# Performance work log

Measured on AMD Instinct MI355X. Metric: run time of the kernel, lower is better.

## Reference

```python
import jax, jax.numpy as jnp
import numpy as np

N_NODES = 50000


def sage_conv(x, src, dst, Wl, bl, Wr):
    # PyG SAGEConv (aggr='mean'): out = lin_l(mean_{j in N(i)} x_j) + lin_r(x_i)
    # lin_l has bias, lin_r (root) has no bias.
    n = x.shape[0]
    agg = jax.ops.segment_sum(x[src], dst, num_segments=n)          # [N, d_in]
    cnt = jax.ops.segment_sum(jnp.ones((src.shape[0],), x.dtype), dst, num_segments=n)
    mean = agg / jnp.maximum(cnt, 1.0)[:, None]
    return mean @ Wl + bl + x @ Wr


def setup_inputs() -> dict:
    key = jax.random.key(0)
    k1, k2, k3, k4, k5, k6, k7 = jax.random.split(key, 7)
    in_c, hid_c, out_c = 128, 128, 2
    x = jax.random.normal(k1, (N_NODES, in_c), dtype=jnp.float32)
    edge_index = jax.random.randint(k2, (2, 800000), 0, N_NODES, dtype=jnp.int64)
    s1 = 1.0 / np.sqrt(in_c)
    s2 = 1.0 / np.sqrt(hid_c)
    return {
        "x": x,
        "edge_index": edge_index,
        "W1l": jax.random.uniform(k3, (in_c, hid_c), jnp.float32, -s1, s1),
        "b1l": jnp.zeros((hid_c,), jnp.float32),
        "W1r": jax.random.uniform(k4, (in_c, hid_c), jnp.float32, -s1, s1),
        "W2l": jax.random.uniform(k5, (hid_c, out_c), jnp.float32, -s2, s2),
        "b2l": jnp.zeros((out_c,), jnp.float32),
        "W2r": jax.random.uniform(k6, (hid_c, out_c), jnp.float32, -s2, s2),
    }


def reference(x, edge_index, W1l, b1l, W1r, W2l, b2l, W2r):
    src, dst = edge_index[0], edge_index[1]
    h = jax.nn.relu(sage_conv(x, src, dst, W1l, b1l, W1r))
    return sage_conv(h, src, dst, W2l, b2l, W2r)
```

## Files before the change

### kernel.cpp

```cpp
#include <hip/hip_runtime.h>

#define N_NODES 50000
#define N_PAD 50176
#define N_EDGES 800000
#define C 128
#define CAP 48
#define BUCK_B 391
#define PACK_B 16
#define TOBF_B 6250

typedef unsigned short ushort_t;
typedef unsigned int uint_t;
typedef __attribute__((ext_vector_type(8))) short bf16x8;
typedef __attribute__((ext_vector_type(4))) float f32x4;

__device__ __forceinline__ uint_t f2bf(float f) {
    uint_t u = __float_as_uint(f);
    u += 0x7fffu + ((u >> 16) & 1u);
    return u >> 16;
}
__device__ __forceinline__ float bflo(uint_t u) { return __uint_as_float(u << 16); }
__device__ __forceinline__ float bfhi(uint_t u) { return __uint_as_float(u & 0xffff0000u); }

__global__ __launch_bounds__(256) void bucketpack_kernel(
    const int* __restrict__ src, const int* __restrict__ dst,
    int* __restrict__ cursor, int* __restrict__ epad,
    const float* __restrict__ W1l, const float* __restrict__ W1r,
    ushort_t* __restrict__ Bp) {
    int b = blockIdx.x;
    if (b < BUCK_B) {
        int i4 = b * 256 + threadIdx.x;
        if (i4 < N_EDGES / 8) {
            int4 s0 = ((const int4*)src)[2 * i4];
            int4 s1 = ((const int4*)src)[2 * i4 + 1];
            int4 d0 = ((const int4*)dst)[2 * i4];
            int4 d1 = ((const int4*)dst)[2 * i4 + 1];
            int p0 = atomicAdd(&cursor[d0.x], 1);
            int p1 = atomicAdd(&cursor[d0.y], 1);
            int p2 = atomicAdd(&cursor[d0.z], 1);
            int p3 = atomicAdd(&cursor[d0.w], 1);
            int p4 = atomicAdd(&cursor[d1.x], 1);
            int p5 = atomicAdd(&cursor[d1.y], 1);
            int p6 = atomicAdd(&cursor[d1.z], 1);
            int p7 = atomicAdd(&cursor[d1.w], 1);
            if (p0 < CAP) epad[d0.x * CAP + p0] = s0.x;
            if (p1 < CAP) epad[d0.y * CAP + p1] = s0.y;
            if (p2 < CAP) epad[d0.z * CAP + p2] = s0.z;
            if (p3 < CAP) epad[d0.w * CAP + p3] = s0.w;
            if (p4 < CAP) epad[d1.x * CAP + p4] = s1.x;
            if (p5 < CAP) epad[d1.y * CAP + p5] = s1.y;
            if (p6 < CAP) epad[d1.z * CAP + p6] = s1.z;
            if (p7 < CAP) epad[d1.w * CAP + p7] = s1.w;
        }
    } else {
        int p = (b - BUCK_B) * 256 + threadIdx.x;
        int lane = p & 63;
        int pair = p >> 6;
        int kk = pair & 7;
        int nt = pair >> 3;
        int n = lane & 15, quad = lane >> 4;
        int col = nt * 16 + n;
        int k0 = kk * 32 + quad * 8;
        uint_t w[4];
        #pragma unroll
        for (int jj = 0; jj < 4; jj++) {
            int ka = k0 + 2 * jj, kb = k0 + 2 * jj + 1;
            float fa = (ka < C) ? W1l[ka * C + col] : W1r[(ka - C) * C + col];
            float fb = (kb < C) ? W1l[kb * C + col] : W1r[(kb - C) * C + col];
            w[jj] = f2bf(fa) | (f2bf(fb) << 16);
        }
        ((uint4*)(Bp + (size_t)p * 8))[0] = make_uint4(w[0], w[1], w[2], w[3]);
    }
}

__global__ __launch_bounds__(256) void tobf16_kernel(const float* __restrict__ x,
                                                     ushort_t* __restrict__ xh) {
    int i = blockIdx.x * 256 + threadIdx.x;
    float4 v = ((const float4*)x)[i];
    uint_t lo = f2bf(v.x) | (f2bf(v.y) << 16);
    uint_t hi = f2bf(v.z) | (f2bf(v.w) << 16);
    ((uint2*)xh)[i] = make_uint2(lo, hi);
}

__device__ __forceinline__ void bf8_acc(float* a, const uint4 v) {
    a[0] += bflo(v.x); a[1] += bfhi(v.x);
    a[2] += bflo(v.y); a[3] += bfhi(v.y);
    a[4] += bflo(v.z); a[5] += bfhi(v.z);
    a[6] += bflo(v.w); a[7] += bfhi(v.w);
}

__global__ __launch_bounds__(256) void gather_kernel(const ushort_t* __restrict__ xh,
                                                     const int* __restrict__ cursor,
                                                     const int* __restrict__ epad,
                                                     ushort_t* __restrict__ msb) {
    int t = threadIdx.x;
    int slot = t >> 4, q = t & 15;
    int node = blockIdx.x * 16 + slot;
    int d = cursor[node];
    int dd = d < CAP ? d : CAP;
    const int* lst = epad + node * CAP;
    float a[8] = {0,0,0,0,0,0,0,0};
    float b[8] = {0,0,0,0,0,0,0,0};
    int e = 0;
    for (; e + 8 <= dd; e += 8) {
        int s0 = lst[e + 0], s1 = lst[e + 1], s2 = lst[e + 2], s3 = lst[e + 3];
        int s4 = lst[e + 4], s5 = lst[e + 5], s6 = lst[e + 6], s7 = lst[e + 7];
        uint4 v0 = ((const uint4*)(xh + (size_t)s0 * C))[q];
        uint4 v1 = ((const uint4*)(xh + (size_t)s1 * C))[q];
        uint4 v2 = ((const uint4*)(xh + (size_t)s2 * C))[q];
        uint4 v3 = ((const uint4*)(xh + (size_t)s3 * C))[q];
        uint4 v4 = ((const uint4*)(xh + (size_t)s4 * C))[q];
        uint4 v5 = ((const uint4*)(xh + (size_t)s5 * C))[q];
        uint4 v6 = ((const uint4*)(xh + (size_t)s6 * C))[q];
        uint4 v7 = ((const uint4*)(xh + (size_t)s7 * C))[q];
        bf8_acc(a, v0); bf8_acc(b, v1); bf8_acc(a, v2); bf8_acc(b, v3);
        bf8_acc(a, v4); bf8_acc(b, v5); bf8_acc(a, v6); bf8_acc(b, v7);
    }
    for (; e + 4 <= dd; e += 4) {
        int s0 = lst[e + 0], s1 = lst[e + 1], s2 = lst[e + 2], s3 = lst[e + 3];
        uint4 v0 = ((const uint4*)(xh + (size_t)s0 * C))[q];
        uint4 v1 = ((const uint4*)(xh + (size_t)s1 * C))[q];
        uint4 v2 = ((const uint4*)(xh + (size_t)s2 * C))[q];
        uint4 v3 = ((const uint4*)(xh + (size_t)s3 * C))[q];
        bf8_acc(a, v0); bf8_acc(b, v1); bf8_acc(a, v2); bf8_acc(b, v3);
    }
    for (; e < dd; e++) {
        uint4 v = ((const uint4*)(xh + (size_t)lst[e] * C))[q];
        bf8_acc(a, v);
    }
    float inv = 1.0f / fmaxf((float)d, 1.0f);
    uint4 o;
    o.x = f2bf((a[0] + b[0]) * inv) | (f2bf((a[1] + b[1]) * inv) << 16);
    o.y = f2bf((a[2] + b[2]) * inv) | (f2bf((a[3] + b[3]) * inv) << 16);
    o.z = f2bf((a[4] + b[4]) * inv) | (f2bf((a[5] + b[5]) * inv) << 16);
    o.w = f2bf((a[6] + b[6]) * inv) | (f2bf((a[7] + b[7]) * inv) << 16);
    ((uint4*)(msb + (size_t)node * C))[q] = o;
}

__global__ __launch_bounds__(512) void gemm_mfma(
    const ushort_t* __restrict__ msb, const ushort_t* __restrict__ xh,
    const ushort_t* __restrict__ Bp, const float* __restrict__ b1l,
    const float* __restrict__ W2l, const float* __restrict__ W2r,
    const float* __restrict__ b2l, float* __restrict__ z, float* __restrict__ out) {
    __shared__ ushort_t sB[2 * C * C];
    int t = threadIdx.x;
    #pragma unroll
    for (int i = 0; i < 8; i++)
        ((uint4*)sB)[i * 512 + t] = ((const uint4*)Bp)[i * 512 + t];
    __syncthreads();

    int wid = t >> 6, lane = t & 63;
    int m = lane & 15, quad = lane >> 4;
    int base = blockIdx.x * 128 + wid * 16;

    const ushort_t* a_ms = msb + (size_t)(base + m) * C + quad * 8;
    const ushort_t* a_xh = xh  + (size_t)(base + m) * C + quad * 8;
    bf16x8 aw[8];
    #pragma unroll
    for (int kk = 0; kk < 4; kk++) aw[kk]     = *(const bf16x8*)(a_ms + kk * 32);
    #pragma unroll
    for (int kk = 0; kk < 4; kk++) aw[4 + kk] = *(const bf16x8*)(a_xh + kk * 32);

    f32x4 acc[8];
    #pragma unroll
    for (int nt = 0; nt < 8; nt++) acc[nt] = (f32x4){0.f, 0.f, 0.f, 0.f};

    const bf16x8* bp = (const bf16x8*)sB;
    #pragma unroll
    for (int kk = 0; kk < 8; kk++) {
        bf16x8 a = aw[kk];
        #pragma unroll
        for (int nt = 0; nt < 8; nt++) {
            bf16x8 bfr = bp[(nt * 8 + kk) * 64 + lane];
            acc[nt] = __builtin_amdgcn_mfma_f32_16x16x32_bf16(a, bfr, acc[nt], 0, 0, 0);
        }
    }

    float zz0[4] = {0,0,0,0}, zz1[4] = {0,0,0,0};
    float rr0[4] = {0,0,0,0}, rr1[4] = {0,0,0,0};
    #pragma unroll
    for (int nt = 0; nt < 8; nt++) {
        int col = nt * 16 + m;
        float bias = b1l[col];
        float2 wl = ((const float2*)W2l)[col];
        float2 wr = ((const float2*)W2r)[col];
        #pragma unroll
        for (int reg = 0; reg < 4; reg++) {
            float h = fmaxf(acc[nt][reg] + bias, 0.0f);
            zz0[reg] = fmaf(h, wl.x, zz0[reg]);
            zz1[reg] = fmaf(h, wl.y, zz1[reg]);
            rr0[reg] = fmaf(h, wr.x, rr0[reg]);
            rr1[reg] = fmaf(h, wr.y, rr1[reg]);
        }
    }
    float bl0 = b2l[0], bl1 = b2l[1];
    #pragma unroll
    for (int reg = 0; reg < 4; reg++) {
        float a0 = zz0[reg], a1 = zz1[reg], c0 = rr0[reg], c1 = rr1[reg];
        #pragma unroll
        for (int off = 8; off > 0; off >>= 1) {
            a0 += __shfl_down(a0, off, 16);
            a1 += __shfl_down(a1, off, 16);
            c0 += __shfl_down(c0, off, 16);
            c1 += __shfl_down(c1, off, 16);
        }
        if (m == 0) {
            int node = base + quad * 4 + reg;
            if (node < N_NODES) {
                z[node * 2 + 0]   = a0;
                z[node * 2 + 1]   = a1;
                out[node * 2 + 0] = c0 + bl0;
                out[node * 2 + 1] = c1 + bl1;
            }
        }
    }
}

__global__ __launch_bounds__(256) void final_kernel(const float* __restrict__ z,
                                                    const int* __restrict__ cursor,
                                                    const int* __restrict__ epad,
                                                    float* __restrict__ out) {
    int t = threadIdx.x;
    int sub = t & 15;
    int node = blockIdx.x * 16 + (t >> 4);
    int d = cursor[node];
    int dd = d < CAP ? d : CAP;
    const int* lst = epad + node * CAP;
    float a0 = 0.0f, a1 = 0.0f;
    for (int e = sub; e < dd; e += 16) {
        float2 v = ((const float2*)z)[lst[e]];
        a0 += v.x; a1 += v.y;
    }
    #pragma unroll
    for (int off = 8; off > 0; off >>= 1) {
        a0 += __shfl_down(a0, off);
        a1 += __shfl_down(a1, off);
    }
    if (sub == 0) {
        float inv = 1.0f / fmaxf((float)d, 1.0f);
        out[node * 2 + 0] += a0 * inv;
        out[node * 2 + 1] += a1 * inv;
    }
}

extern "C" void kernel_launch(void* const* d_in, const int* in_sizes, int n_in,
                              void* d_out, int out_size, void* d_ws, size_t ws_size,
                              hipStream_t stream) {
    const float* x   = (const float*)d_in[0];
    const int*   ei  = (const int*)d_in[1];
    const float* W1l = (const float*)d_in[2];
    const float* b1l = (const float*)d_in[3];
    const float* W1r = (const float*)d_in[4];
    const float* W2l = (const float*)d_in[5];
    const float* b2l = (const float*)d_in[6];
    const float* W2r = (const float*)d_in[7];
    float* out = (float*)d_out;

    const int* src = ei;
    const int* dst = ei + N_EDGES;

    int* cursor   = (int*)d_ws;
    int* epad     = cursor + N_PAD;
    ushort_t* xh  = (ushort_t*)(epad + N_NODES * CAP);
    ushort_t* msb = xh + (size_t)N_PAD * C;
    ushort_t* Bp  = msb + (size_t)N_PAD * C;
    float* z      = (float*)(Bp + 2 * C * C);

    hipMemsetAsync(cursor, 0, N_NODES * sizeof(int), stream);

    bucketpack_kernel<<<BUCK_B + PACK_B, 256, 0, stream>>>(
        src, dst, cursor, epad, W1l, W1r, Bp);
    tobf16_kernel<<<TOBF_B, 256, 0, stream>>>(x, xh);
    gather_kernel<<<N_NODES / 16, 256, 0, stream>>>(xh, cursor, epad, msb);
    gemm_mfma<<<392, 512, 0, stream>>>(
        msb, xh, Bp, b1l, W2l, W2r, b2l, z, out);
    final_kernel<<<N_NODES / 16, 256, 0, stream>>>(z, cursor, epad, out);
}
```

Baseline: 176.1 us.

## Replace per-node global atomic bucketing with two-pass coarse/fine bucket sort

New measurement: 157.8 us. -10.4%, faster.

```diff
diff --git a/kernel.cpp b/kernel.cpp
--- a/kernel.cpp
+++ b/kernel.cpp
@@ -5,9 +5,11 @@
 #define N_EDGES 800000
 #define C 128
 #define CAP 48
-#define BUCK_B 391
+#define NB 196
+#define CBCAP 4608
+#define B1_BUCK 391
+#define TOBF_B 6250
 #define PACK_B 16
-#define TOBF_B 6250
 
 typedef unsigned short ushort_t;
 typedef unsigned int uint_t;
@@ -22,38 +24,83 @@
 __device__ __forceinline__ float bflo(uint_t u) { return __uint_as_float(u << 16); }
 __device__ __forceinline__ float bfhi(uint_t u) { return __uint_as_float(u & 0xffff0000u); }
 
-__global__ __launch_bounds__(256) void bucketpack_kernel(
+__global__ __launch_bounds__(256) void bucket1_kernel(
     const int* __restrict__ src, const int* __restrict__ dst,
+    int* __restrict__ gcur, int2* __restrict__ cb,
+    const float* __restrict__ x, ushort_t* __restrict__ xh) {
+    int b = blockIdx.x;
+    if (b < B1_BUCK) {
+        __shared__ int hist[NB];
+        __shared__ int offs[NB];
+        int t = threadIdx.x;
+        if (t < NB) hist[t] = 0;
+        __syncthreads();
+        int tid = b * 256 + t;
+        bool act = tid < N_EDGES / 8;
+        int4 s0, s1, d0, d1;
+        if (act) {
+            s0 = ((const int4*)src)[2 * tid];
+            s1 = ((const int4*)src)[2 * tid + 1];
+            d0 = ((const int4*)dst)[2 * tid];
+            d1 = ((const int4*)dst)[2 * tid + 1];
+            atomicAdd(&hist[d0.x >> 8], 1);
+            atomicAdd(&hist[d0.y >> 8], 1);
+            atomicAdd(&hist[d0.z >> 8], 1);
+            atomicAdd(&hist[d0.w >> 8], 1);
+            atomicAdd(&hist[d1.x >> 8], 1);
+            atomicAdd(&hist[d1.y >> 8], 1);
+            atomicAdd(&hist[d1.z >> 8], 1);
+            atomicAdd(&hist[d1.w >> 8], 1);
+        }
+        __syncthreads();
+        if (t < NB) {
+            offs[t] = atomicAdd(&gcur[t], hist[t]);
+            hist[t] = 0;
+        }
+        __syncthreads();
+        if (act) {
+            int ss[8] = {s0.x, s0.y, s0.z, s0.w, s1.x, s1.y, s1.z, s1.w};
+            int dd[8] = {d0.x, d0.y, d0.z, d0.w, d1.x, d1.y, d1.z, d1.w};
+            #pragma unroll
+            for (int i = 0; i < 8; i++) {
+                int bkt = dd[i] >> 8;
+                int pos = offs[bkt] + atomicAdd(&hist[bkt], 1);
+                if (pos < CBCAP) cb[bkt * CBCAP + pos] = make_int2(ss[i], dd[i]);
+            }
+        }
+    } else {
+        int i = (b - B1_BUCK) * 256 + threadIdx.x;
+        float4 v = ((const float4*)x)[i];
+        uint_t lo = f2bf(v.x) | (f2bf(v.y) << 16);
+        uint_t hi = f2bf(v.z) | (f2bf(v.w) << 16);
+        ((uint2*)xh)[i] = make_uint2(lo, hi);
+    }
+}
+
+__global__ __launch_bounds__(256) void bucket2_kernel(
+    const int* __restrict__ gcur, const int2* __restrict__ cb,
     int* __restrict__ cursor, int* __restrict__ epad,
     const float* __restrict__ W1l, const float* __restrict__ W1r,
     ushort_t* __restrict__ Bp) {
     int b = blockIdx.x;
-    if (b < BUCK_B) {
-        int i4 = b * 256 + threadIdx.x;
-        if (i4 < N_EDGES / 8) {
-            int4 s0 = ((const int4*)src)[2 * i4];
-            int4 s1 = ((const int4*)src)[2 * i4 + 1];
-            int4 d0 = ((const int4*)dst)[2 * i4];
-            int4 d1 = ((const int4*)dst)[2 * i4 + 1];
-            int p0 = atomicAdd(&cursor[d0.x], 1);
-            int p1 = atomicAdd(&cursor[d0.y], 1);
-            int p2 = atomicAdd(&cursor[d0.z], 1);
-            int p3 = atomicAdd(&cursor[d0.w], 1);
-            int p4 = atomicAdd(&cursor[d1.x], 1);
-            int p5 = atomicAdd(&cursor[d1.y], 1);
-            int p6 = atomicAdd(&cursor[d1.z], 1);
-            int p7 = atomicAdd(&cursor[d1.w], 1);
-            if (p0 < CAP) epad[d0.x * CAP + p0] = s0.x;
-            if (p1 < CAP) epad[d0.y * CAP + p1] = s0.y;
-            if (p2 < CAP) epad[d0.z * CAP + p2] = s0.z;
-            if (p3 < CAP) epad[d0.w * CAP + p3] = s0.w;
-            if (p4 < CAP) epad[d1.x * CAP + p4] = s1.x;
-            if (p5 < CAP) epad[d1.y * CAP + p5] = s1.y;
-            if (p6 < CAP) epad[d1.z * CAP + p6] = s1.z;
-            if (p7 < CAP) epad[d1.w * CAP + p7] = s1.w;
-        }
+    if (b < NB) {
+        __shared__ int cnt[256];
+        int t = threadIdx.x;
+        cnt[t] = 0;
+        __syncthreads();
+        int lenr = gcur[b];
+        int len = lenr < CBCAP ? lenr : CBCAP;
+        const int2* run = cb + b * CBCAP;
+        for (int e = t; e < len; e += 256) {
+            int2 sd = run[e];
+            int pos = atomicAdd(&cnt[sd.y & 255], 1);
+            if (pos < CAP) epad[sd.y * CAP + pos] = sd.x;
+        }
+        __syncthreads();
+        int node = b * 256 + t;
+        if (node < N_NODES) cursor[node] = cnt[t];
     } else {
-        int p = (b - BUCK_B) * 256 + threadIdx.x;
+        int p = (b - NB) * 256 + threadIdx.x;
         int lane = p & 63;
         int pair = p >> 6;
         int kk = pair & 7;
@@ -71,15 +118,6 @@
         }
         ((uint4*)(Bp + (size_t)p * 8))[0] = make_uint4(w[0], w[1], w[2], w[3]);
     }
-}
-
-__global__ __launch_bounds__(256) void tobf16_kernel(const float* __restrict__ x,
-                                                     ushort_t* __restrict__ xh) {
-    int i = blockIdx.x * 256 + threadIdx.x;
-    float4 v = ((const float4*)x)[i];
-    uint_t lo = f2bf(v.x) | (f2bf(v.y) << 16);
-    uint_t hi = f2bf(v.z) | (f2bf(v.w) << 16);
-    ((uint2*)xh)[i] = make_uint2(lo, hi);
 }
 
 __device__ __forceinline__ void bf8_acc(float* a, const uint4 v) {
@@ -259,20 +297,20 @@
     const int* src = ei;
     const int* dst = ei + N_EDGES;
 
-    int* cursor   = (int*)d_ws;
+    int* gcur     = (int*)d_ws;
+    int2* cb      = (int2*)(gcur + 256);
+    int* cursor   = (int*)(cb + NB * CBCAP);
     int* epad     = cursor + N_PAD;
     ushort_t* xh  = (ushort_t*)(epad + N_NODES * CAP);
     ushort_t* msb = xh + (size_t)N_PAD * C;
     ushort_t* Bp  = msb + (size_t)N_PAD * C;
     float* z      = (float*)(Bp + 2 * C * C);
 
-    hipMemsetAsync(cursor, 0, N_NODES * sizeof(int), stream);
-
-    bucketpack_kernel<<<BUCK_B + PACK_B, 256, 0, stream>>>(
-        src, dst, cursor, epad, W1l, W1r, Bp);
-    tobf16_kernel<<<TOBF_B, 256, 0, stream>>>(x, xh);
+    hipMemsetAsync(gcur, 0, NB * sizeof(int), stream);
+
+    bucket1_kernel<<<B1_BUCK + TOBF_B, 256, 0, stream>>>(src, dst, gcur, cb, x, xh);
+    bucket2_kernel<<<NB + PACK_B, 256, 0, stream>>>(gcur, cb, cursor, epad, W1l, W1r, Bp);
     gather_kernel<<<N_NODES / 16, 256, 0, stream>>>(xh, cursor, epad, msb);
-    gemm_mfma<<<392, 512, 0, stream>>>(
-        msb, xh, Bp, b1l, W2l, W2r, b2l, z, out);
+    gemm_mfma<<<392, 512, 0, stream>>>(msb, xh, Bp, b1l, W2l, W2r, b2l, z, out);
     final_kernel<<<N_NODES / 16, 256, 0, stream>>>(z, cursor, epad, out);
 }
```
